# Optimization experiments

Hardware: AMD Instinct MI355X
Metric: run time of the kernel (lower is better)

The kernel has to match this reference:

```python
import jax, jax.numpy as jnp
import numpy as np

L = 4        # num_layers
H = 1024     # hidden_size
NH = 16      # num_heads
KVH = 4      # num_kv_heads
QPK = NH // KVH
HD = H // NH # head_dim = 64
FF = 4096    # intermediate_size
V = 32000    # vocab_size
B, S = 2, 2048
EPS = 1e-5
STD = 0.02


def layernorm(x, g, b):
    m = jnp.mean(x, axis=-1, keepdims=True)
    v = jnp.mean(jnp.square(x - m), axis=-1, keepdims=True)
    return (x - m) * jax.lax.rsqrt(v + EPS) * g + b


def setup_inputs() -> dict:
    key = jax.random.key(0)
    ks = iter(jax.random.split(key, 24))
    n = lambda shape: STD * jax.random.normal(next(ks), shape, dtype=jnp.float32)
    KV = H * KVH // NH  # kv_size = 256
    inp = {
        'input_ids': jax.random.randint(next(ks), (B, S), 0, V),
        'attention_mask': jnp.zeros((B, S), dtype=jnp.float32),
        'tok_emb': n((V, H)),
        'pos_emb': n((S, H)),
        # per-layer stacked weights, stored [in, out] so y = x @ W + b
        'Wq': n((L, H, H)),  'bq': jnp.zeros((L, H)),
        'Wk': n((L, H, KV)), 'bk': jnp.zeros((L, KV)),
        'Wv': n((L, H, KV)), 'bv': jnp.zeros((L, KV)),
        'Wo': n((L, H, H)),  'bo': jnp.zeros((L, H)),
        'W1': n((L, H, FF)), 'b1': jnp.zeros((L, FF)),
        'W2': n((L, FF, H)), 'b2': jnp.zeros((L, H)),
        'ln1_g': jnp.ones((L, H)), 'ln1_b': jnp.zeros((L, H)),
        'ln2_g': jnp.ones((L, H)), 'ln2_b': jnp.zeros((L, H)),
        'lnf_g': jnp.ones((H,)),   'lnf_b': jnp.zeros((H,)),
        'Whead': n((H, V)),  # head has no bias
    }
    return inp


def gpt_forward(input_ids, attention_mask, tok_emb, pos_emb,
                Wq, bq, Wk, bk, Wv, bv, Wo, bo,
                W1, b1, W2, b2, ln1_g, ln1_b, ln2_g, ln2_b,
                lnf_g, lnf_b, Whead):
    b, s = input_ids.shape
    x = tok_emb[input_ids] + pos_emb[None, :s, :]  # [b,s,H]
    mask = attention_mask[:, None, None, None, :]  # [b,1,1,1,s] additive
    scale = 1.0 / jnp.sqrt(jnp.float32(HD))
    for l in range(L):
        h = layernorm(x, ln1_g[l], ln1_b[l])
        q = h @ Wq[l] + bq[l]                              # [b,s,H]
        k = h @ Wk[l] + bk[l]                              # [b,s,KV]
        v = h @ Wv[l] + bv[l]
        q = q.reshape(b, s, KVH, QPK, HD).transpose(0, 2, 3, 1, 4)  # [b,g,q,s,d]
        k = k.reshape(b, s, KVH, HD).transpose(0, 2, 1, 3)          # [b,g,s,d]
        v = v.reshape(b, s, KVH, HD).transpose(0, 2, 1, 3)
        scores = jnp.einsum('bgqsd,bgkd->bgqsk', q, k) * scale      # [b,g,q,s,s]
        scores = scores + mask
        w = jax.nn.softmax(scores, axis=-1)
        o = jnp.einsum('bgqsk,bgkd->bgqsd', w, v)                   # [b,g,q,s,d]
        o = o.transpose(0, 3, 1, 2, 4).reshape(b, s, H)
        x = x + (o @ Wo[l] + bo[l])
        h2 = layernorm(x, ln2_g[l], ln2_b[l])
        ff = jax.nn.gelu(h2 @ W1[l] + b1[l], approximate=False) @ W2[l] + b2[l]
        x = x + ff
    x = layernorm(x, lnf_g, lnf_b)
    return x @ Whead  # [b,s,V] logits


def reference(input_ids, attention_mask, tok_emb, pos_emb,
              Wq, bq, Wk, bk, Wv, bv, Wo, bo,
              W1, b1, W2, b2, ln1_g, ln1_b, ln2_g, ln2_b,
              lnf_g, lnf_b, Whead):
    return gpt_forward(input_ids, attention_mask, tok_emb, pos_emb,
                       Wq, bq, Wk, bk, Wv, bv, Wo, bo,
                       W1, b1, W2, b2, ln1_g, ln1_b, ln2_g, ln2_b,
                       lnf_g, lnf_b, Whead)
```

## Files before the change

### kernel.cpp

```cpp
#include <hip/hip_runtime.h>
#include <hip/hip_bf16.h>

#define LAYERS 4
#define H 1024
#define NH 16
#define KVH 4
#define HD 64
#define KVD 256
#define FF 4096
#define VOC 32000
#define BB 2
#define SS 2048
#define MROWS (BB*SS)
#define QKVN 1536

typedef __attribute__((ext_vector_type(4))) float f32x4;
typedef __attribute__((ext_vector_type(8))) short short8;
typedef __attribute__((ext_vector_type(4))) unsigned short u16x4;
typedef __attribute__((ext_vector_type(2))) unsigned int u32x2;

__device__ inline unsigned short f2bf(float f){
  union { float f; unsigned u; } v; v.f = f;
  return (unsigned short)((v.u + 0x7FFFu + ((v.u >> 16) & 1u)) >> 16);
}
__device__ inline unsigned cvt_pk_bf16(float a, float b){
  unsigned r;
  asm("v_cvt_pk_bf16_f32 %0, %1, %2" : "=v"(r) : "v"(a), "v"(b));
  return r;
}

__global__ __launch_bounds__(256) void embed_kernel(const int* __restrict__ ids,
    const float* __restrict__ tok, const float* __restrict__ pos, float* __restrict__ x)
{
  int row = blockIdx.x;
  int s = row & (SS-1);
  int id = ids[row];
  int t = threadIdx.x;
  f32x4 a = *(const f32x4*)&tok[(size_t)id*H + t*4];
  f32x4 p = *(const f32x4*)&pos[(size_t)s*H + t*4];
  *(f32x4*)&x[(size_t)row*H + t*4] = a + p;
}

__global__ __launch_bounds__(256) void ln_kernel(const float* __restrict__ x,
    const float* __restrict__ g, const float* __restrict__ b, unsigned short* __restrict__ out)
{
  int row = blockIdx.x;
  int t = threadIdx.x;
  const float* xr = x + (size_t)row*H;
  f32x4 v = *(const f32x4*)&xr[t*4];
  float s  = v[0]+v[1]+v[2]+v[3];
  float s2 = v[0]*v[0]+v[1]*v[1]+v[2]*v[2]+v[3]*v[3];
  #pragma unroll
  for (int off=1; off<64; off<<=1){ s += __shfl_xor(s,off); s2 += __shfl_xor(s2,off); }
  __shared__ float red[8];
  int w = t>>6;
  if ((t&63)==0){ red[w]=s; red[4+w]=s2; }
  __syncthreads();
  float S1 = red[0]+red[1]+red[2]+red[3];
  float S2 = red[4]+red[5]+red[6]+red[7];
  float mean = S1 * (1.0f/H);
  float var  = S2 * (1.0f/H) - mean*mean;
  float rs = rsqrtf(var + 1e-5f);
  u16x4 o;
  #pragma unroll
  for (int i=0;i<4;i++) o[i] = f2bf((v[i]-mean)*rs*g[t*4+i] + b[t*4+i]);
  *(u16x4*)&out[(size_t)row*H + t*4] = o;
}

__global__ __launch_bounds__(256) void convT_kernel(const float* __restrict__ in,
    unsigned short* __restrict__ out, int K, int N, size_t istride, size_t ostride)
{
  __shared__ float t[32][33];
  in  += (size_t)blockIdx.z * istride;
  out += (size_t)blockIdx.z * ostride;
  int n0 = blockIdx.x*32, k0 = blockIdx.y*32;
  int x = threadIdx.x & 31, y = threadIdx.x >> 5;
  #pragma unroll
  for (int j=0;j<4;j++) t[y+j*8][x] = in[(size_t)(k0+y+j*8)*N + n0 + x];
  __syncthreads();
  int x2 = threadIdx.x & 15, y2 = threadIdx.x >> 4;
  #pragma unroll
  for (int j=0;j<2;j++){
    int n = y2 + j*16;
    unsigned lo = f2bf(t[x2*2][n]);
    unsigned hi = f2bf(t[x2*2+1][n]);
    *(unsigned*)&out[(size_t)(n0+n)*K + k0 + x2*2] = lo | (hi<<16);
  }
}

__global__ __launch_bounds__(256) void bcat_kernel(const float* __restrict__ bq,
    const float* __restrict__ bk, const float* __restrict__ bv, float* __restrict__ out)
{
  int l = blockIdx.x, t = threadIdx.x;
  #pragma unroll
  for (int i=0;i<4;i++) out[l*QKVN + t + i*256] = bq[l*H + t + i*256];
  out[l*QKVN + 1024 + t] = bk[l*KVD + t];
  out[l*QKVN + 1280 + t] = bv[l*KVD + t];
}

template<int EPI>
__global__ __launch_bounds__(256, 2) void gemm_bt(
    const unsigned short* __restrict__ A, const unsigned short* __restrict__ Bt,
    const float* __restrict__ bias, const float* __restrict__ res,
    float* __restrict__ outf, unsigned short* __restrict__ outb,
    unsigned short* __restrict__ outb2, unsigned short* __restrict__ outb3, int N, int K)
{
  __shared__ __align__(16) char lds[65536];
  const int tid = threadIdx.x;
  const int lane = tid & 63, wid = tid >> 6;
  const int wr = (wid>>1)*64, wc = (wid&1)*64;
  const int fr = lane & 15, fq = lane >> 4;
  const int m0 = blockIdx.x*128, n0 = blockIdx.y*128;
  const int nt = K >> 5;
  f32x4 acc[4][4] = {};

  #define STG1(PTR, baserow, kt, ldsoff) do {                                   \
    _Pragma("unroll")                                                           \
    for (int c=0;c<2;c++){                                                      \
      int rr = c*64 + (tid>>2);                                                 \
      int ss = (tid&3) ^ ((rr>>1)&3);                                           \
      __builtin_amdgcn_global_load_lds(                                         \
        (const __attribute__((address_space(1))) void*)((PTR) + (size_t)((baserow)+rr)*K + (kt)*32 + ss*8), \
        (__attribute__((address_space(3))) void*)(lds + (ldsoff) + c*4096 + wid*1024), 16, 0, 0); \
    }                                                                           \
  } while(0)
  #define RDA1(buf,row) (*(const short8*)(lds + (buf)*16384 + (row)*64 + ((fq ^ (((row)>>1)&3))*16)))
  #define RDB1(buf,row) (*(const short8*)(lds + (buf)*16384 + 8192 + (row)*64 + ((fq ^ (((row)>>1)&3))*16)))

  STG1(A,  m0, 0, 0);      STG1(Bt, n0, 0, 8192);
  STG1(A,  m0, 1, 16384);  STG1(Bt, n0, 1, 16384+8192);
  STG1(A,  m0, 2, 32768);  STG1(Bt, n0, 2, 32768+8192);
  asm volatile("s_waitcnt vmcnt(8)" ::: "memory");
  __builtin_amdgcn_s_barrier();

  for (int t = 0; t < nt; ++t){
    const int buf = t & 3;
    const int s3 = (t+3) & 3;
    const int t3 = (t+3 < nt) ? t+3 : t;
    short8 af[4], bf[4];
    #pragma unroll
    for (int mi=0;mi<4;mi++) af[mi] = RDA1(buf, wr+mi*16+fr);
    #pragma unroll
    for (int ni=0;ni<4;ni++) bf[ni] = RDB1(buf, wc+ni*16+fr);
    STG1(A,  m0, t3, s3*16384);
    STG1(Bt, n0, t3, s3*16384+8192);
    __builtin_amdgcn_s_barrier();
    asm volatile("s_waitcnt lgkmcnt(0)" ::: "memory");
    __builtin_amdgcn_s_setprio(1);
    #pragma unroll
    for (int mi=0;mi<4;mi++)
      #pragma unroll
      for (int ni=0;ni<4;ni++)
        acc[mi][ni] = __builtin_amdgcn_mfma_f32_16x16x32_bf16(af[mi], bf[ni], acc[mi][ni], 0,0,0);
    __builtin_amdgcn_s_setprio(0);
    asm volatile("s_waitcnt vmcnt(8)" ::: "memory");
    __builtin_amdgcn_s_barrier();
  }
  #undef STG1
  #undef RDA1
  #undef RDB1

  #pragma unroll
  for (int mi=0;mi<4;mi++)
    #pragma unroll
    for (int ni=0;ni<4;ni++){
      int col = n0 + wc + ni*16 + fr;
      float bi = (EPI==3) ? 0.0f : bias[col];
      #pragma unroll
      for (int r=0;r<4;r++){
        int row = m0 + wr + mi*16 + fq*4 + r;
        float vv = acc[mi][ni][r] + bi;
        if (EPI==1)      { size_t idx=(size_t)row*N+col; outf[idx] = vv + res[idx]; }
        else if (EPI==2) { size_t idx=(size_t)row*N+col; outb[idx] = f2bf(0.5f*vv*(1.0f+erff(vv*0.70710678118f))); }
        else if (EPI==3) { size_t idx=(size_t)row*N+col; outf[idx] = vv; }
        else if (EPI==5) {
          if (col < 1024)      outb [(size_t)row*H + col]            = f2bf(vv);
          else if (col < 1280) outb2[(size_t)row*KVD + (col-1024)]   = f2bf(vv);
          else                 outb3[(size_t)(col-1280)*MROWS + row] = f2bf(vv);
        }
      }
    }
}

template<int EPI>
__global__ __launch_bounds__(512, 2) void gemm256(
    const unsigned short* __restrict__ A, const unsigned short* __restrict__ Bt,
    const float* __restrict__ bias, float* __restrict__ outf,
    unsigned short* __restrict__ outb, int N, int K)
{
  __shared__ __align__(16) char lds[131072];
  const int tid = threadIdx.x;
  const int lane = tid & 63, wid = tid >> 6;
  const int wrr = wid >> 2, wc = wid & 3;
  const int fr = lane & 15, fq = lane >> 4;
  const int m0 = blockIdx.x*256, n0 = blockIdx.y*256;
  const int nt = K >> 5;
  f32x4 acc[8][4] = {};

  #define STG(PTR, baserow, kt, ldsoff) do {                                    \
    _Pragma("unroll")                                                           \
    for (int c=0;c<2;c++){                                                      \
      int rr = c*128 + (tid>>2);                                                \
      int ss = (tid&3) ^ ((rr>>1)&3);                                           \
      __builtin_amdgcn_global_load_lds(                                         \
        (const __attribute__((address_space(1))) void*)((PTR) + (size_t)((baserow)+rr)*K + (kt)*32 + ss*8), \
        (__attribute__((address_space(3))) void*)(lds + (ldsoff) + c*8192 + wid*1024), 16, 0, 0); \
    }                                                                           \
  } while(0)
  #define RDA(buf,row) (*(const short8*)(lds + (buf)*32768 + (row)*64 + ((fq ^ (((row)>>1)&3))*16)))
  #define RDB(buf,row) (*(const short8*)(lds + (buf)*32768 + 16384 + (row)*64 + ((fq ^ (((row)>>1)&3))*16)))

  STG(A,  m0, 0, 0);      STG(Bt, n0, 0, 16384);
  STG(A,  m0, 1, 32768);  STG(Bt, n0, 1, 32768+16384);
  STG(A,  m0, 2, 65536);  STG(Bt, n0, 2, 65536+16384);
  asm volatile("s_waitcnt vmcnt(8)" ::: "memory");
  __builtin_amdgcn_s_barrier();

  short8 a[4], b2[2];
  short8 bA = RDB(0, wc*64+fr);
  short8 bB = RDB(0, wc*64+16+fr);
  #pragma unroll
  for (int mi=0;mi<4;mi++) a[mi] = RDA(0, wrr*128+mi*16+fr);

  for (int t = 0; t < nt; ++t){
    const int buf = t & 3;
    const int s3 = (t+3) & 3;
    const int nb = (t+1) & 3;
    const int t3 = (t+3 < nt) ? t+3 : nt-1;
    short8 ah[4];
    #pragma unroll
    for (int mi=0;mi<4;mi++) ah[mi] = RDA(buf, wrr*128+(4+mi)*16+fr);
    b2[0] = RDB(buf, wc*64+32+fr);
    b2[1] = RDB(buf, wc*64+48+fr);
    STG(A, m0, t3, s3*32768);
    __builtin_amdgcn_s_setprio(1);
    #pragma unroll
    for (int mi=0;mi<4;mi++){
      acc[mi][0] = __builtin_amdgcn_mfma_f32_16x16x32_bf16(a[mi], bA, acc[mi][0], 0,0,0);
      acc[mi][1] = __builtin_amdgcn_mfma_f32_16x16x32_bf16(a[mi], bB, acc[mi][1], 0,0,0);
    }
    __builtin_amdgcn_s_setprio(0);
    STG(Bt, n0, t3, s3*32768+16384);
    __builtin_amdgcn_s_setprio(1);
    #pragma unroll
    for (int mi=0;mi<4;mi++){
      acc[4+mi][0] = __builtin_amdgcn_mfma_f32_16x16x32_bf16(ah[mi], bA, acc[4+mi][0], 0,0,0);
      acc[4+mi][1] = __builtin_amdgcn_mfma_f32_16x16x32_bf16(ah[mi], bB, acc[4+mi][1], 0,0,0);
    }
    __builtin_amdgcn_s_setprio(0);
    asm volatile("s_waitcnt lgkmcnt(0)" ::: "memory");
    asm volatile("s_waitcnt vmcnt(8)" ::: "memory");
    __builtin_amdgcn_s_barrier();
    short8 nbA = RDB(nb, wc*64+fr);
    short8 nbB = RDB(nb, wc*64+16+fr);
    short8 na[4];
    #pragma unroll
    for (int mi=0;mi<4;mi++) na[mi] = RDA(nb, wrr*128+mi*16+fr);
    __builtin_amdgcn_s_setprio(1);
    #pragma unroll
    for (int mi=0;mi<4;mi++){
      acc[mi][2] = __builtin_amdgcn_mfma_f32_16x16x32_bf16(a[mi], b2[0], acc[mi][2], 0,0,0);
      acc[mi][3] = __builtin_amdgcn_mfma_f32_16x16x32_bf16(a[mi], b2[1], acc[mi][3], 0,0,0);
    }
    __builtin_amdgcn_s_setprio(0);
    __builtin_amdgcn_s_setprio(1);
    #pragma unroll
    for (int mi=0;mi<4;mi++){
      acc[4+mi][2] = __builtin_amdgcn_mfma_f32_16x16x32_bf16(ah[mi], b2[0], acc[4+mi][2], 0,0,0);
      acc[4+mi][3] = __builtin_amdgcn_mfma_f32_16x16x32_bf16(ah[mi], b2[1], acc[4+mi][3], 0,0,0);
    }
    __builtin_amdgcn_s_setprio(0);
    bA = nbA; bB = nbB;
    #pragma unroll
    for (int mi=0;mi<4;mi++) a[mi] = na[mi];
  }
  #undef STG
  #undef RDA
  #undef RDB

  #pragma unroll
  for (int mi=0; mi<8; mi++)
    #pragma unroll
    for (int ni=0; ni<4; ni++){
      int col = n0 + wc*64 + ni*16 + fr;
      float bi = (EPI==3) ? 0.0f : bias[col];
      #pragma unroll
      for (int r=0; r<4; r++){
        int row = m0 + wrr*128 + mi*16 + fq*4 + r;
        float vv = acc[mi][ni][r] + bi;
        size_t idx = (size_t)row*N + col;
        if (EPI==3) outf[idx] = vv;
        else        outb[idx] = f2bf(0.5f*vv*(1.0f+erff(vv*0.70710678118f)));
      }
    }
}

#define LOG2E 1.4426950408889634f
__global__ __launch_bounds__(256) void attn_kernel(
    const unsigned short* __restrict__ q, const unsigned short* __restrict__ kptr,
    const unsigned short* __restrict__ vt, const float* __restrict__ mask,
    unsigned short* __restrict__ o)
{
  __shared__ char Pbuf[4][4096];
  int tid = threadIdx.x;
  int lane = tid & 63, wid = tid >> 6;
  int fr = lane & 15, fq = lane >> 4, fo = fq*8;
  int h = blockIdx.y, b = blockIdx.z, g = h >> 2;
  int qcol = h*HD, kcol = g*HD;
  int qbase = b*SS + blockIdx.x*128 + wid*32;
  char* Pl = Pbuf[wid];
  int swz = (fr & 7) << 4;

  short8 bq[2][2];
  #pragma unroll
  for (int h2=0; h2<2; h2++){
    const unsigned short* qrow = q + (size_t)(qbase + h2*16 + fr)*H + qcol;
    bq[h2][0] = *(const short8*)(qrow + fo);
    bq[h2][1] = *(const short8*)(qrow + 32 + fo);
  }

  f32x4 oacc[2][4] = {};
  float mrun[2] = {-1e30f, -1e30f}, lsum[2] = {0.f, 0.f};
  const float sc2 = 0.125f * LOG2E;

  const unsigned short* kp[4];
  #pragma unroll
  for (int f=0; f<4; f++) kp[f] = kptr + (size_t)(b*SS + f*16 + fr)*KVD + kcol + fo;
  const unsigned short* vp[4];
  #pragma unroll
  for (int dc=0; dc<4; dc++) vp[dc] = vt + (size_t)(kcol + dc*16 + fr)*MROWS + b*SS + fo;
  const float* mp = mask + b*SS + fq*4;

  short8 kaA[4][2], kaB[4][2];
  #pragma unroll
  for (int f=0; f<4; f++){
    kaA[f][0] = *(const short8*)(kp[f]);
    kaA[f][1] = *(const short8*)(kp[f] + 32);
    kp[f] += 64*KVD;
  }

#define ATTN_STEP(KA, KB, PF) do {                                             \
    f32x4 mkv[4];                                                              \
    _Pragma("unroll")                                                          \
    for (int f=0; f<4; f++) mkv[f] = *(const f32x4*)(mp + f*16);               \
    short8 va[4][2];                                                           \
    _Pragma("unroll")                                                          \
    for (int dc=0; dc<4; dc++){                                                \
      va[dc][0] = *(const short8*)(vp[dc]);                                    \
      va[dc][1] = *(const short8*)(vp[dc] + 32);                               \
    }                                                                          \
    f32x4 sf[2][4] = {};                                                       \
    __builtin_amdgcn_s_setprio(1);                                             \
    _Pragma("unroll")                                                          \
    for (int h2=0; h2<2; h2++)                                                 \
      _Pragma("unroll")                                                        \
      for (int f=0; f<4; f++){                                                 \
        sf[h2][f] = __builtin_amdgcn_mfma_f32_16x16x32_bf16(KA[f][0], bq[h2][0], sf[h2][f],0,0,0); \
        sf[h2][f] = __builtin_amdgcn_mfma_f32_16x16x32_bf16(KA[f][1], bq[h2][1], sf[h2][f],0,0,0); \
      }                                                                        \
    __builtin_amdgcn_s_setprio(0);                                             \
    if (PF){                                                                   \
      _Pragma("unroll")                                                        \
      for (int f=0; f<4; f++){                                                 \
        KB[f][0] = *(const short8*)(kp[f]);                                    \
        KB[f][1] = *(const short8*)(kp[f] + 32);                               \
        kp[f] += 64*KVD;                                                       \
      }                                                                        \
    }                                                                          \
    _Pragma("unroll")                                                          \
    for (int f=0; f<4; f++){                                                   \
      _Pragma("unroll")                                                        \
      for (int r=0; r<4; r++){                                                 \
        float m2 = mkv[f][r]*LOG2E;                                            \
        sf[0][f][r] = sf[0][f][r]*sc2 + m2;                                    \
        sf[1][f][r] = sf[1][f][r]*sc2 + m2;                                    \
      }                                                                        \
    }                                                                          \
    float pm[2];                                                               \
    _Pragma("unroll")                                                          \
    for (int h2=0; h2<2; h2++){                                                \
      float a0 = fmaxf(fmaxf(sf[h2][0][0],sf[h2][0][1]), fmaxf(sf[h2][0][2],sf[h2][0][3])); \
      float a1 = fmaxf(fmaxf(sf[h2][1][0],sf[h2][1][1]), fmaxf(sf[h2][1][2],sf[h2][1][3])); \
      float a2 = fmaxf(fmaxf(sf[h2][2][0],sf[h2][2][1]), fmaxf(sf[h2][2][2],sf[h2][2][3])); \
      float a3 = fmaxf(fmaxf(sf[h2][3][0],sf[h2][3][1]), fmaxf(sf[h2][3][2],sf[h2][3][3])); \
      float p = fmaxf(fmaxf(a0,a1), fmaxf(a2,a3));                             \
      p = fmaxf(p, __shfl_xor(p, 16));                                         \
      p = fmaxf(p, __shfl_xor(p, 32));                                         \
      pm[h2] = p;                                                              \
    }                                                                          \
    if (!__all(pm[0] <= mrun[0]+8.f && pm[1] <= mrun[1]+8.f)){                 \
      float al[2];                                                             \
      _Pragma("unroll")                                                        \
      for (int h2=0; h2<2; h2++){                                              \
        float mn = fmaxf(mrun[h2], pm[h2]);                                    \
        al[h2] = __builtin_amdgcn_exp2f(mrun[h2]-mn);                          \
        mrun[h2] = mn;                                                         \
        lsum[h2] *= al[h2];                                                    \
      }                                                                        \
      _Pragma("unroll")                                                        \
      for (int r=0; r<4; r++){                                                 \
        float altl = __shfl(al[0], fq*4+r);                                    \
        float alth = __shfl(al[1], fq*4+r);                                    \
        _Pragma("unroll")                                                      \
        for (int dc=0; dc<4; dc++){ oacc[0][dc][r]*=altl; oacc[1][dc][r]*=alth; } \
      }                                                                        \
    }                                                                          \
    _Pragma("unroll")                                                          \
    for (int h2=0; h2<2; h2++){                                                \
      float ps = 0.f;                                                          \
      _Pragma("unroll")                                                        \
      for (int f=0; f<4; f++)                                                  \
        _Pragma("unroll")                                                      \
        for (int r=0; r<4; r++){                                               \
          float e = __builtin_amdgcn_exp2f(sf[h2][f][r]-mrun[h2]);             \
          sf[h2][f][r] = e; ps += e;                                           \
        }                                                                      \
      ps += __shfl_xor(ps, 16);                                                \
      ps += __shfl_xor(ps, 32);                                                \
      lsum[h2] += ps;                                                          \
    }                                                                          \
    _Pragma("unroll")                                                          \
    for (int h2=0; h2<2; h2++){                                                \
      int prow = h2*16 + fr;                                                   \
      _Pragma("unroll")                                                        \
      for (int f=0; f<4; f++){                                                 \
        u32x2 pw;                                                              \
        pw[0] = cvt_pk_bf16(sf[h2][f][0], sf[h2][f][1]);                       \
        pw[1] = cvt_pk_bf16(sf[h2][f][2], sf[h2][f][3]);                       \
        *(u32x2*)(Pl + prow*128 + ((f*32 + fq*8) ^ swz)) = pw;                 \
      }                                                                        \
    }                                                                          \
    __builtin_amdgcn_s_setprio(1);                                             \
    _Pragma("unroll")                                                          \
    for (int h2=0; h2<2; h2++){                                                \
      int prow = h2*16 + fr;                                                   \
      _Pragma("unroll")                                                        \
      for (int gs=0; gs<2; gs++){                                              \
        short8 pa = *(const short8*)(Pl + prow*128 + ((gs*64 + fq*16) ^ swz)); \
        _Pragma("unroll")                                                      \
        for (int dc=0; dc<4; dc++)                                             \
          oacc[h2][dc] = __builtin_amdgcn_mfma_f32_16x16x32_bf16(pa, va[dc][gs], oacc[h2][dc],0,0,0); \
      }                                                                        \
    }                                                                          \
    __builtin_amdgcn_s_setprio(0);                                             \
    _Pragma("unroll")                                                          \
    for (int dc=0; dc<4; dc++) vp[dc] += 64;                                   \
    mp += 64;                                                                  \
  } while(0)

  for (int it = 0; it < SS/128 - 1; ++it){
    ATTN_STEP(kaA, kaB, 1);
    ATTN_STEP(kaB, kaA, 1);
  }
  ATTN_STEP(kaA, kaB, 1);
  ATTN_STEP(kaB, kaA, 0);
#undef ATTN_STEP

  #pragma unroll
  for (int h2=0; h2<2; h2++){
    float lt[4];
    #pragma unroll
    for (int r=0; r<4; r++) lt[r] = __shfl(lsum[h2], fq*4+r);
    #pragma unroll
    for (int dc=0; dc<4; dc++)
      #pragma unroll
      for (int r=0; r<4; r++){
        int row = qbase + h2*16 + fq*4 + r;
        o[(size_t)row*H + qcol + dc*16 + fr] = f2bf(oacc[h2][dc][r] / lt[r]);
      }
  }
}

extern "C" void kernel_launch(void* const* d_in, const int* in_sizes, int n_in,
                              void* d_out, int out_size, void* d_ws, size_t ws_size,
                              hipStream_t stream)
{
  const int*   ids  = (const int*)  d_in[0];
  const float* mask = (const float*)d_in[1];
  const float* tok  = (const float*)d_in[2];
  const float* pos  = (const float*)d_in[3];
  const float* Wq   = (const float*)d_in[4];
  const float* bq   = (const float*)d_in[5];
  const float* Wk   = (const float*)d_in[6];
  const float* bk   = (const float*)d_in[7];
  const float* Wv   = (const float*)d_in[8];
  const float* bv   = (const float*)d_in[9];
  const float* Wo   = (const float*)d_in[10];
  const float* bo   = (const float*)d_in[11];
  const float* W1   = (const float*)d_in[12];
  const float* b1   = (const float*)d_in[13];
  const float* W2   = (const float*)d_in[14];
  const float* b2   = (const float*)d_in[15];
  const float* ln1g = (const float*)d_in[16];
  const float* ln1b = (const float*)d_in[17];
  const float* ln2g = (const float*)d_in[18];
  const float* ln2b = (const float*)d_in[19];
  const float* lnfg = (const float*)d_in[20];
  const float* lnfb = (const float*)d_in[21];
  const float* Wh   = (const float*)d_in[22];
  float* out = (float*)d_out;

  char* ws = (char*)d_ws;
  float*          x    = (float*)ws;          ws += (size_t)MROWS*H*4;
  unsigned short* hb   = (unsigned short*)ws; ws += (size_t)MROWS*H*2;
  unsigned short* qb   = (unsigned short*)ws; ws += (size_t)MROWS*H*2;
  unsigned short* kb   = (unsigned short*)ws; ws += (size_t)MROWS*KVD*2;
  unsigned short* vtb  = (unsigned short*)ws; ws += (size_t)KVD*MROWS*2;
  unsigned short* ob   = (unsigned short*)ws; ws += (size_t)MROWS*H*2;
  unsigned short* f1   = (unsigned short*)ws; ws += (size_t)MROWS*FF*2;
  unsigned short* Wqkv = (unsigned short*)ws; ws += (size_t)LAYERS*QKVN*H*2;
  unsigned short* WoT  = (unsigned short*)ws; ws += (size_t)LAYERS*H*H*2;
  unsigned short* W1T  = (unsigned short*)ws; ws += (size_t)LAYERS*H*FF*2;
  unsigned short* W2T  = (unsigned short*)ws; ws += (size_t)LAYERS*H*FF*2;
  unsigned short* WhT  = (unsigned short*)ws; ws += (size_t)H*VOC*2;
  float*          bcat = (float*)ws;          ws += (size_t)LAYERS*QKVN*4;

  convT_kernel<<<dim3(H/32,   H/32,  LAYERS), 256, 0, stream>>>(Wq, Wqkv,          H,  H,   (size_t)H*H,   (size_t)QKVN*H);
  convT_kernel<<<dim3(KVD/32, H/32,  LAYERS), 256, 0, stream>>>(Wk, Wqkv + 1024*H, H,  KVD, (size_t)H*KVD, (size_t)QKVN*H);
  convT_kernel<<<dim3(KVD/32, H/32,  LAYERS), 256, 0, stream>>>(Wv, Wqkv + 1280*H, H,  KVD, (size_t)H*KVD, (size_t)QKVN*H);
  convT_kernel<<<dim3(H/32,   H/32,  LAYERS), 256, 0, stream>>>(Wo, WoT,           H,  H,   (size_t)H*H,   (size_t)H*H);
  convT_kernel<<<dim3(FF/32,  H/32,  LAYERS), 256, 0, stream>>>(W1, W1T,           H,  FF,  (size_t)H*FF,  (size_t)H*FF);
  convT_kernel<<<dim3(H/32,   FF/32, LAYERS), 256, 0, stream>>>(W2, W2T,           FF, H,   (size_t)FF*H,  (size_t)FF*H);
  convT_kernel<<<dim3(VOC/32, H/32,  1),      256, 0, stream>>>(Wh, WhT,           H,  VOC, 0, 0);
  bcat_kernel<<<LAYERS, 256, 0, stream>>>(bq, bk, bv, bcat);

  embed_kernel<<<MROWS, 256, 0, stream>>>(ids, tok, pos, x);
  for (int l=0; l<LAYERS; l++){
    ln_kernel<<<MROWS,256,0,stream>>>(x, ln1g + l*H, ln1b + l*H, hb);
    gemm_bt<5><<<dim3(MROWS/128, QKVN/128),256,0,stream>>>(hb, Wqkv + (size_t)l*QKVN*H, bcat + l*QKVN, nullptr, nullptr, qb, kb, vtb, QKVN, H);
    attn_kernel<<<dim3(SS/128, NH, BB), 256, 0, stream>>>(qb, kb, vtb, mask, ob);
    gemm_bt<1><<<dim3(MROWS/128, H/128),  256,0,stream>>>(ob, WoT + (size_t)l*H*H,  bo + l*H,  x, x, nullptr, nullptr, nullptr, H, H);
    ln_kernel<<<MROWS,256,0,stream>>>(x, ln2g + l*H, ln2b + l*H, hb);
    gemm256<2><<<dim3(MROWS/256, FF/256), 512,0,stream>>>(hb, W1T + (size_t)l*H*FF, b1 + l*FF, nullptr, f1, FF, H);
    gemm_bt<1><<<dim3(MROWS/128, H/128),  256,0,stream>>>(f1, W2T + (size_t)l*H*FF, b2 + l*H,  x, x, nullptr, nullptr, nullptr, H, FF);
  }
  ln_kernel<<<MROWS,256,0,stream>>>(x, lnfg, lnfb, hb);
  gemm256<3><<<dim3(MROWS/256, VOC/256), 512,0,stream>>>(hb, WhT, nullptr, out, nullptr, VOC, H);
}
```

Baseline: 1.665 ms.

## Software-pipeline LDS fragment reads with MFMA in the GEMM main loop

Restructures the GEMM k-loop so the A fragments and half of the B fragments for the next tile are read from LDS while MFMAs for the current tile are still issuing. The MFMAs are split into two halves interleaved with LDS reads, and one barrier per iteration is removed. The goal is to hide LDS read latency behind matrix-core work. The cost is more live registers for the double-buffered fragments, which may lower occupancy. A read of buffer (t+1)&3 on the last iteration may touch stale data, but that data is never used.

```diff
diff --git a/kernel.cpp b/kernel.cpp
--- a/kernel.cpp
+++ b/kernel.cpp
@@ -133,28 +133,46 @@
   asm volatile("s_waitcnt vmcnt(8)" ::: "memory");
   __builtin_amdgcn_s_barrier();
 
+  short8 a[4], b01[2], b23[2];
+  #pragma unroll
+  for (int mi=0;mi<4;mi++) a[mi] = RDA1(0, wr+mi*16+fr);
+  b01[0] = RDB1(0, wc+fr);
+  b01[1] = RDB1(0, wc+16+fr);
+
   for (int t = 0; t < nt; ++t){
     const int buf = t & 3;
     const int s3 = (t+3) & 3;
-    const int t3 = (t+3 < nt) ? t+3 : t;
-    short8 af[4], bf[4];
-    #pragma unroll
-    for (int mi=0;mi<4;mi++) af[mi] = RDA1(buf, wr+mi*16+fr);
-    #pragma unroll
-    for (int ni=0;ni<4;ni++) bf[ni] = RDB1(buf, wc+ni*16+fr);
+    const int nb = (t+1) & 3;
+    const int t3 = (t+3 < nt) ? t+3 : nt-1;
+    b23[0] = RDB1(buf, wc+32+fr);
+    b23[1] = RDB1(buf, wc+48+fr);
     STG1(A,  m0, t3, s3*16384);
     STG1(Bt, n0, t3, s3*16384+8192);
-    __builtin_amdgcn_s_barrier();
+    __builtin_amdgcn_s_setprio(1);
+    #pragma unroll
+    for (int mi=0;mi<4;mi++){
+      acc[mi][0] = __builtin_amdgcn_mfma_f32_16x16x32_bf16(a[mi], b01[0], acc[mi][0], 0,0,0);
+      acc[mi][1] = __builtin_amdgcn_mfma_f32_16x16x32_bf16(a[mi], b01[1], acc[mi][1], 0,0,0);
+    }
+    __builtin_amdgcn_s_setprio(0);
     asm volatile("s_waitcnt lgkmcnt(0)" ::: "memory");
-    __builtin_amdgcn_s_setprio(1);
-    #pragma unroll
-    for (int mi=0;mi<4;mi++)
-      #pragma unroll
-      for (int ni=0;ni<4;ni++)
-        acc[mi][ni] = __builtin_amdgcn_mfma_f32_16x16x32_bf16(af[mi], bf[ni], acc[mi][ni], 0,0,0);
-    __builtin_amdgcn_s_setprio(0);
     asm volatile("s_waitcnt vmcnt(8)" ::: "memory");
     __builtin_amdgcn_s_barrier();
+    short8 na[4], nb01[2];
+    nb01[0] = RDB1(nb, wc+fr);
+    nb01[1] = RDB1(nb, wc+16+fr);
+    #pragma unroll
+    for (int mi=0;mi<4;mi++) na[mi] = RDA1(nb, wr+mi*16+fr);
+    __builtin_amdgcn_s_setprio(1);
+    #pragma unroll
+    for (int mi=0;mi<4;mi++){
+      acc[mi][2] = __builtin_amdgcn_mfma_f32_16x16x32_bf16(a[mi], b23[0], acc[mi][2], 0,0,0);
+      acc[mi][3] = __builtin_amdgcn_mfma_f32_16x16x32_bf16(a[mi], b23[1], acc[mi][3], 0,0,0);
+    }
+    __builtin_amdgcn_s_setprio(0);
+    b01[0] = nb01[0]; b01[1] = nb01[1];
+    #pragma unroll
+    for (int mi=0;mi<4;mi++) a[mi] = na[mi];
   }
   #undef STG1
   #undef RDA1
```

Result: no change. 1.667 ms (+0.1%).

## Use 8-wave gemm_bt blocks with register double-buffered fragments and one barrier

Applied to the files above, without the earlier changes.

Reworks the 128x128 gemm_bt kernel to run 8 waves per block instead of 4, with each wave computing a 64x32 sub-tile. The main loop now prefetches the next k-step's LDS fragments into registers, interleaved between two halves of the MFMA work, and drops from two barriers per iteration to one. The goal is to hide LDS read and barrier latency and raise wave-level parallelism for the QKV, Wo and W2 GEMMs. The cost is lower per-wave register reuse, meaning more LDS reads per MFMA. The launch bound of 4 blocks cannot be met, because 64KB of LDS per block limits occupancy.

```diff
diff --git a/kernel.cpp b/kernel.cpp
--- a/kernel.cpp
+++ b/kernel.cpp
@@ -99,7 +99,7 @@
 }
 
 template<int EPI>
-__global__ __launch_bounds__(256, 2) void gemm_bt(
+__global__ __launch_bounds__(512, 4) void gemm_bt(
     const unsigned short* __restrict__ A, const unsigned short* __restrict__ Bt,
     const float* __restrict__ bias, const float* __restrict__ res,
     float* __restrict__ outf, unsigned short* __restrict__ outb,
@@ -108,21 +108,18 @@
   __shared__ __align__(16) char lds[65536];
   const int tid = threadIdx.x;
   const int lane = tid & 63, wid = tid >> 6;
-  const int wr = (wid>>1)*64, wc = (wid&1)*64;
+  const int wr = (wid>>2)*64, wc = (wid&3)*32;
   const int fr = lane & 15, fq = lane >> 4;
   const int m0 = blockIdx.x*128, n0 = blockIdx.y*128;
   const int nt = K >> 5;
-  f32x4 acc[4][4] = {};
+  f32x4 acc[4][2] = {};
 
   #define STG1(PTR, baserow, kt, ldsoff) do {                                   \
-    _Pragma("unroll")                                                           \
-    for (int c=0;c<2;c++){                                                      \
-      int rr = c*64 + (tid>>2);                                                 \
-      int ss = (tid&3) ^ ((rr>>1)&3);                                           \
-      __builtin_amdgcn_global_load_lds(                                         \
-        (const __attribute__((address_space(1))) void*)((PTR) + (size_t)((baserow)+rr)*K + (kt)*32 + ss*8), \
-        (__attribute__((address_space(3))) void*)(lds + (ldsoff) + c*4096 + wid*1024), 16, 0, 0); \
-    }                                                                           \
+    int rr = tid>>2;                                                            \
+    int ss = (tid&3) ^ ((rr>>1)&3);                                             \
+    __builtin_amdgcn_global_load_lds(                                           \
+      (const __attribute__((address_space(1))) void*)((PTR) + (size_t)((baserow)+rr)*K + (kt)*32 + ss*8), \
+      (__attribute__((address_space(3))) void*)(lds + (ldsoff) + wid*1024), 16, 0, 0); \
   } while(0)
   #define RDA1(buf,row) (*(const short8*)(lds + (buf)*16384 + (row)*64 + ((fq ^ (((row)>>1)&3))*16)))
   #define RDB1(buf,row) (*(const short8*)(lds + (buf)*16384 + 8192 + (row)*64 + ((fq ^ (((row)>>1)&3))*16)))
@@ -130,31 +127,42 @@
   STG1(A,  m0, 0, 0);      STG1(Bt, n0, 0, 8192);
   STG1(A,  m0, 1, 16384);  STG1(Bt, n0, 1, 16384+8192);
   STG1(A,  m0, 2, 32768);  STG1(Bt, n0, 2, 32768+8192);
-  asm volatile("s_waitcnt vmcnt(8)" ::: "memory");
+  asm volatile("s_waitcnt vmcnt(4)" ::: "memory");
   __builtin_amdgcn_s_barrier();
 
+  short8 a[4], b[2];
+  #pragma unroll
+  for (int mi=0;mi<4;mi++) a[mi] = RDA1(0, wr+mi*16+fr);
+  b[0] = RDB1(0, wc+fr);
+  b[1] = RDB1(0, wc+16+fr);
+
   for (int t = 0; t < nt; ++t){
-    const int buf = t & 3;
     const int s3 = (t+3) & 3;
-    const int t3 = (t+3 < nt) ? t+3 : t;
-    short8 af[4], bf[4];
-    #pragma unroll
-    for (int mi=0;mi<4;mi++) af[mi] = RDA1(buf, wr+mi*16+fr);
-    #pragma unroll
-    for (int ni=0;ni<4;ni++) bf[ni] = RDB1(buf, wc+ni*16+fr);
+    const int nb = (t+1) & 3;
+    const int t3 = (t+3 < nt) ? t+3 : nt-1;
     STG1(A,  m0, t3, s3*16384);
     STG1(Bt, n0, t3, s3*16384+8192);
+    __builtin_amdgcn_s_setprio(1);
+    #pragma unroll
+    for (int mi=0;mi<4;mi++)
+      acc[mi][0] = __builtin_amdgcn_mfma_f32_16x16x32_bf16(a[mi], b[0], acc[mi][0], 0,0,0);
+    __builtin_amdgcn_s_setprio(0);
+    asm volatile("s_waitcnt lgkmcnt(0)" ::: "memory");
+    asm volatile("s_waitcnt vmcnt(4)" ::: "memory");
     __builtin_amdgcn_s_barrier();
-    asm volatile("s_waitcnt lgkmcnt(0)" ::: "memory");
+    short8 na[4], nb0, nb1;
+    nb0 = RDB1(nb, wc+fr);
+    nb1 = RDB1(nb, wc+16+fr);
+    #pragma unroll
+    for (int mi=0;mi<4;mi++) na[mi] = RDA1(nb, wr+mi*16+fr);
     __builtin_amdgcn_s_setprio(1);
     #pragma unroll
     for (int mi=0;mi<4;mi++)
-      #pragma unroll
-      for (int ni=0;ni<4;ni++)
-        acc[mi][ni] = __builtin_amdgcn_mfma_f32_16x16x32_bf16(af[mi], bf[ni], acc[mi][ni], 0,0,0);
+      acc[mi][1] = __builtin_amdgcn_mfma_f32_16x16x32_bf16(a[mi], b[1], acc[mi][1], 0,0,0);
     __builtin_amdgcn_s_setprio(0);
-    asm volatile("s_waitcnt vmcnt(8)" ::: "memory");
-    __builtin_amdgcn_s_barrier();
+    b[0] = nb0; b[1] = nb1;
+    #pragma unroll
+    for (int mi=0;mi<4;mi++) a[mi] = na[mi];
   }
   #undef STG1
   #undef RDA1
@@ -163,7 +171,7 @@
   #pragma unroll
   for (int mi=0;mi<4;mi++)
     #pragma unroll
-    for (int ni=0;ni<4;ni++){
+    for (int ni=0;ni<2;ni++){
       int col = n0 + wc + ni*16 + fr;
       float bi = (EPI==3) ? 0.0f : bias[col];
       #pragma unroll
@@ -527,12 +535,12 @@
   embed_kernel<<<MROWS, 256, 0, stream>>>(ids, tok, pos, x);
   for (int l=0; l<LAYERS; l++){
     ln_kernel<<<MROWS,256,0,stream>>>(x, ln1g + l*H, ln1b + l*H, hb);
-    gemm_bt<5><<<dim3(MROWS/128, QKVN/128),256,0,stream>>>(hb, Wqkv + (size_t)l*QKVN*H, bcat + l*QKVN, nullptr, nullptr, qb, kb, vtb, QKVN, H);
+    gemm_bt<5><<<dim3(MROWS/128, QKVN/128),512,0,stream>>>(hb, Wqkv + (size_t)l*QKVN*H, bcat + l*QKVN, nullptr, nullptr, qb, kb, vtb, QKVN, H);
     attn_kernel<<<dim3(SS/128, NH, BB), 256, 0, stream>>>(qb, kb, vtb, mask, ob);
-    gemm_bt<1><<<dim3(MROWS/128, H/128),  256,0,stream>>>(ob, WoT + (size_t)l*H*H,  bo + l*H,  x, x, nullptr, nullptr, nullptr, H, H);
+    gemm_bt<1><<<dim3(MROWS/128, H/128),  512,0,stream>>>(ob, WoT + (size_t)l*H*H,  bo + l*H,  x, x, nullptr, nullptr, nullptr, H, H);
     ln_kernel<<<MROWS,256,0,stream>>>(x, ln2g + l*H, ln2b + l*H, hb);
     gemm256<2><<<dim3(MROWS/256, FF/256), 512,0,stream>>>(hb, W1T + (size_t)l*H*FF, b1 + l*FF, nullptr, f1, FF, H);
-    gemm_bt<1><<<dim3(MROWS/128, H/128),  256,0,stream>>>(f1, W2T + (size_t)l*H*FF, b2 + l*H,  x, x, nullptr, nullptr, nullptr, H, FF);
+    gemm_bt<1><<<dim3(MROWS/128, H/128),  512,0,stream>>>(f1, W2T + (size_t)l*H*FF, b2 + l*H,  x, x, nullptr, nullptr, nullptr, H, FF);
   }
   ln_kernel<<<MROWS,256,0,stream>>>(x, lnfg, lnfb, hb);
   gemm256<3><<<dim3(MROWS/256, VOC/256), 512,0,stream>>>(hb, WhT, nullptr, out, nullptr, VOC, H);
```

Result: no change. 1.675 ms (+0.6%).
